# Optimization experiments

Hardware: AMD Instinct MI355X
Metric: run time of the kernel (lower is better)

The kernel has to match this reference:

```python
import jax, jax.numpy as jnp
import numpy as np

S, B, D, CAND = 256, 512, 1024, 1024  # seq_len, batch, mem_dim, cand_dim


def setup_inputs() -> dict:
    key = jax.random.key(0)
    k1, k2, k3, k4 = jax.random.split(key, 4)
    M = jax.random.normal(k1, (S, B, D), dtype=jnp.float32)
    x = jax.random.normal(k2, (B, CAND), dtype=jnp.float32)
    mask = jnp.ones((B, S), dtype=jnp.float32)
    W = jax.random.normal(k3, (D, CAND), dtype=jnp.float32) * 0.02  # nn.Linear weight
    b = jax.random.normal(k4, (D,), dtype=jnp.float32) * 0.02
    return {"M": M, "x": x, "mask": mask, "W": W, "b": b}


def reference(M, x, mask, W, b):
    # M: (S, B, D), x: (B, CAND), mask: (B, S)
    x_ = x @ W.T + b                          # (B, D) -- transform(x)
    Mb = jnp.transpose(M, (1, 2, 0))          # (B, D, S) -- M.permute(1,2,0)
    Mm = Mb * mask[:, None, :]                # mask memory along seq
    alpha_ = jnp.einsum('bd,bds->bs', x_, Mm) * mask  # (B, S) scores, masked
    alpha_ = jnp.tanh(alpha_)
    alpha_ = jax.nn.softmax(alpha_, axis=1)
    am = alpha_ * mask                        # re-mask after softmax
    alpha = am / jnp.sum(am, axis=1, keepdims=True)   # renormalize
    attn_pool = jnp.einsum('bs,sbd->bd', alpha, M)    # (B, D)
    return attn_pool, alpha[:, None, :]       # alpha as (B, 1, S) like torch
```

## Files before the change

### kernel.cpp

```cpp
#include <hip/hip_runtime.h>
#include <hip/hip_bf16.h>
#include <math.h>

#define S_LEN 256
#define B_SZ  512
#define D_DIM 1024
#define CAND_ 1024

#define TB 32
#define TD 64
#define TK 32

__launch_bounds__(256, 2)
__global__ void transform_gemm(const float* __restrict__ x,
                               const float* __restrict__ W,
                               const float* __restrict__ bias,
                               float* __restrict__ xw) {
    __shared__ float xt[TK][TB + 2];
    __shared__ float wt[TK][TD + 4];

    const int b0 = blockIdx.x * TB;
    const int d0 = blockIdx.y * TD;
    const int t  = threadIdx.x;
    const int td = t & 15;
    const int tb = t >> 4;

    float acc0[4] = {0.f, 0.f, 0.f, 0.f};
    float acc1[4] = {0.f, 0.f, 0.f, 0.f};

    const int xr  = t >> 3;
    const int xkc = t & 7;

    for (int k0 = 0; k0 < CAND_; k0 += TK) {
        {
            float4 xv = *(const float4*)&x[(size_t)(b0 + xr) * CAND_ + k0 + xkc * 4];
            xt[xkc * 4 + 0][xr] = xv.x;
            xt[xkc * 4 + 1][xr] = xv.y;
            xt[xkc * 4 + 2][xr] = xv.z;
            xt[xkc * 4 + 3][xr] = xv.w;
        }
        #pragma unroll
        for (int h = 0; h < 2; ++h) {
            int c   = t + h * 256;
            int wr  = c >> 3;
            int wkc = c & 7;
            float4 wv = *(const float4*)&W[(size_t)(d0 + wr) * CAND_ + k0 + wkc * 4];
            wt[wkc * 4 + 0][wr] = wv.x;
            wt[wkc * 4 + 1][wr] = wv.y;
            wt[wkc * 4 + 2][wr] = wv.z;
            wt[wkc * 4 + 3][wr] = wv.w;
        }
        __syncthreads();
        #pragma unroll
        for (int k = 0; k < TK; ++k) {
            float2 xa = *(const float2*)&xt[k][tb * 2];
            float4 wv = *(const float4*)&wt[k][td * 4];
            acc0[0] = fmaf(xa.x, wv.x, acc0[0]);
            acc0[1] = fmaf(xa.x, wv.y, acc0[1]);
            acc0[2] = fmaf(xa.x, wv.z, acc0[2]);
            acc0[3] = fmaf(xa.x, wv.w, acc0[3]);
            acc1[0] = fmaf(xa.y, wv.x, acc1[0]);
            acc1[1] = fmaf(xa.y, wv.y, acc1[1]);
            acc1[2] = fmaf(xa.y, wv.z, acc1[2]);
            acc1[3] = fmaf(xa.y, wv.w, acc1[3]);
        }
        __syncthreads();
    }

    const float4 bv = *(const float4*)&bias[d0 + td * 4];
    const int b = b0 + tb * 2;
    const int d = d0 + td * 4;
    float4 o0 = {acc0[0] + bv.x, acc0[1] + bv.y, acc0[2] + bv.z, acc0[3] + bv.w};
    float4 o1 = {acc1[0] + bv.x, acc1[1] + bv.y, acc1[2] + bv.z, acc1[3] + bv.w};
    *(float4*)&xw[(size_t)b * D_DIM + d]       = o0;
    *(float4*)&xw[(size_t)(b + 1) * D_DIM + d] = o1;
}

#define NW 8
#define NS (S_LEN / NW)

__launch_bounds__(512, 2)
__global__ void fused_attn(const float* __restrict__ M,
                           const float* __restrict__ mask,
                           const float* __restrict__ xw,
                           float* __restrict__ out) {
    __shared__ float s_acc[NW][D_DIM];
    __shared__ float s_w[S_LEN];
    __shared__ float s_den[NW];

    const int b    = blockIdx.x;
    const int tid  = threadIdx.x;
    const int lane = tid & 63;
    const int wv   = tid >> 6;

    const float4* xp = (const float4*)(xw + (size_t)b * D_DIM);
    const float4 x0 = xp[lane];
    const float4 x1 = xp[lane + 64];
    const float4 x2 = xp[lane + 128];
    const float4 x3 = xp[lane + 192];

    const float* mrow = mask + (size_t)b * S_LEN;

    float4 a0 = {0, 0, 0, 0}, a1 = {0, 0, 0, 0}, a2 = {0, 0, 0, 0}, a3 = {0, 0, 0, 0};
    float denom = 0.f;

    const int s_begin = wv * NS;
    const float4* rp = (const float4*)(M + ((size_t)s_begin * B_SZ + b) * D_DIM);
    float4 c0 = rp[lane];
    float4 c1 = rp[lane + 64];
    float4 c2 = rp[lane + 128];
    float4 c3 = rp[lane + 192];

    for (int i = 0; i < NS; ++i) {
        const int s = s_begin + i;
        float4 n0 = c0, n1 = c1, n2 = c2, n3 = c3;
        if (i + 1 < NS) {
            const float4* np = (const float4*)(M + ((size_t)(s + 1) * B_SZ + b) * D_DIM);
            n0 = np[lane];
            n1 = np[lane + 64];
            n2 = np[lane + 128];
            n3 = np[lane + 192];
        }
        float p = c0.x * x0.x;
        p = fmaf(c0.y, x0.y, p); p = fmaf(c0.z, x0.z, p); p = fmaf(c0.w, x0.w, p);
        p = fmaf(c1.x, x1.x, p); p = fmaf(c1.y, x1.y, p); p = fmaf(c1.z, x1.z, p);
        p = fmaf(c1.w, x1.w, p); p = fmaf(c2.x, x2.x, p); p = fmaf(c2.y, x2.y, p);
        p = fmaf(c2.z, x2.z, p); p = fmaf(c2.w, x2.w, p); p = fmaf(c3.x, x3.x, p);
        p = fmaf(c3.y, x3.y, p); p = fmaf(c3.z, x3.z, p); p = fmaf(c3.w, x3.w, p);
        #pragma unroll
        for (int off = 32; off > 0; off >>= 1)
            p += __shfl_xor(p, off, 64);

        const float mk    = mrow[s];
        const float score = p * mk * mk;
        const float w     = mk * expf(tanhf(score));
        denom += w;
        if (lane == 0) s_w[s] = w;

        a0.x = fmaf(w, c0.x, a0.x); a0.y = fmaf(w, c0.y, a0.y);
        a0.z = fmaf(w, c0.z, a0.z); a0.w = fmaf(w, c0.w, a0.w);
        a1.x = fmaf(w, c1.x, a1.x); a1.y = fmaf(w, c1.y, a1.y);
        a1.z = fmaf(w, c1.z, a1.z); a1.w = fmaf(w, c1.w, a1.w);
        a2.x = fmaf(w, c2.x, a2.x); a2.y = fmaf(w, c2.y, a2.y);
        a2.z = fmaf(w, c2.z, a2.z); a2.w = fmaf(w, c2.w, a2.w);
        a3.x = fmaf(w, c3.x, a3.x); a3.y = fmaf(w, c3.y, a3.y);
        a3.z = fmaf(w, c3.z, a3.z); a3.w = fmaf(w, c3.w, a3.w);

        c0 = n0; c1 = n1; c2 = n2; c3 = n3;
    }

    float* sa = &s_acc[wv][0];
    ((float4*)sa)[lane]       = a0;
    ((float4*)sa)[lane + 64]  = a1;
    ((float4*)sa)[lane + 128] = a2;
    ((float4*)sa)[lane + 192] = a3;
    if (lane == 0) s_den[wv] = denom;
    __syncthreads();

    float dtot = 0.f;
    #pragma unroll
    for (int w8 = 0; w8 < NW; ++w8) dtot += s_den[w8];
    const float inv = 1.0f / dtot;

    #pragma unroll
    for (int j = 0; j < 2; ++j) {
        const int d = tid * 2 + j;
        float v = 0.f;
        #pragma unroll
        for (int w8 = 0; w8 < NW; ++w8) v += s_acc[w8][d];
        out[(size_t)b * D_DIM + d] = v * inv;
    }
    if (tid < S_LEN) {
        out[(size_t)B_SZ * D_DIM + (size_t)b * S_LEN + tid] = s_w[tid] * inv;
    }
}

extern "C" void kernel_launch(void* const* d_in, const int* in_sizes, int n_in,
                              void* d_out, int out_size, void* d_ws, size_t ws_size,
                              hipStream_t stream) {
    const float* M    = (const float*)d_in[0];
    const float* x    = (const float*)d_in[1];
    const float* mask = (const float*)d_in[2];
    const float* W    = (const float*)d_in[3];
    const float* bias = (const float*)d_in[4];
    float* out = (float*)d_out;

    const size_t xw_bytes = (size_t)B_SZ * D_DIM * sizeof(float);
    float* xw = (ws_size >= xw_bytes) ? (float*)d_ws : out;

    dim3 ggrid(B_SZ / TB, D_DIM / TD);
    transform_gemm<<<ggrid, 256, 0, stream>>>(x, W, bias, xw);
    fused_attn<<<B_SZ, 512, 0, stream>>>(M, mask, xw, out);
}
```

Baseline: 729.5 us.

## Split-K the transform GEMM and unroll attention loop to two rows per step

The transform GEMM is split along K into two partial outputs written to workspace, which doubles grid parallelism. The attention kernel sums the two partials when it loads x. The attention loop now handles two sequence rows per iteration with independent dot-product chains and interleaved shuffle reductions. The mask is staged in shared memory and launch bounds are raised to four blocks per CU. This raises register pressure from double-buffering eight float4 rows and adds a second partial-buffer write and read.

Result: slower. 754.7 us (+3.5%).

```diff
diff --git a/kernel.cpp b/kernel.cpp
--- a/kernel.cpp
+++ b/kernel.cpp
@@ -15,12 +15,17 @@
 __global__ void transform_gemm(const float* __restrict__ x,
                                const float* __restrict__ W,
                                const float* __restrict__ bias,
-                               float* __restrict__ xw) {
+                               float* __restrict__ xwp,
+                               int ksplit) {
     __shared__ float xt[TK][TB + 2];
     __shared__ float wt[TK][TD + 4];
 
     const int b0 = blockIdx.x * TB;
     const int d0 = blockIdx.y * TD;
+    const int kz = blockIdx.z;
+    const int kspan = CAND_ / ksplit;
+    const int kbase = kz * kspan;
+
     const int t  = threadIdx.x;
     const int td = t & 15;
     const int tb = t >> 4;
@@ -31,7 +36,7 @@
     const int xr  = t >> 3;
     const int xkc = t & 7;
 
-    for (int k0 = 0; k0 < CAND_; k0 += TK) {
+    for (int k0 = kbase; k0 < kbase + kspan; k0 += TK) {
         {
             float4 xv = *(const float4*)&x[(size_t)(b0 + xr) * CAND_ + k0 + xkc * 4];
             xt[xkc * 4 + 0][xr] = xv.x;
@@ -67,25 +72,63 @@
         __syncthreads();
     }
 
-    const float4 bv = *(const float4*)&bias[d0 + td * 4];
+    float bx = 0.f, by = 0.f, bz = 0.f, bw = 0.f;
+    if (kz == 0) {
+        const float4 bv = *(const float4*)&bias[d0 + td * 4];
+        bx = bv.x; by = bv.y; bz = bv.z; bw = bv.w;
+    }
     const int b = b0 + tb * 2;
     const int d = d0 + td * 4;
-    float4 o0 = {acc0[0] + bv.x, acc0[1] + bv.y, acc0[2] + bv.z, acc0[3] + bv.w};
-    float4 o1 = {acc1[0] + bv.x, acc1[1] + bv.y, acc1[2] + bv.z, acc1[3] + bv.w};
-    *(float4*)&xw[(size_t)b * D_DIM + d]       = o0;
-    *(float4*)&xw[(size_t)(b + 1) * D_DIM + d] = o1;
+    float* dst = xwp + (size_t)kz * B_SZ * D_DIM;
+    float4 o0 = {acc0[0] + bx, acc0[1] + by, acc0[2] + bz, acc0[3] + bw};
+    float4 o1 = {acc1[0] + bx, acc1[1] + by, acc1[2] + bz, acc1[3] + bw};
+    *(float4*)&dst[(size_t)b * D_DIM + d]       = o0;
+    *(float4*)&dst[(size_t)(b + 1) * D_DIM + d] = o1;
 }
 
 #define NW 8
 #define NS (S_LEN / NW)
 
-__launch_bounds__(512, 2)
+#define LOAD_ROW(r0, r1, r2, r3, sidx)                                        \
+    do {                                                                      \
+        const float4* _p = (const float4*)(M + ((size_t)(sidx) * B_SZ + b) * D_DIM); \
+        r0 = _p[lane]; r1 = _p[lane + 64]; r2 = _p[lane + 128]; r3 = _p[lane + 192]; \
+    } while (0)
+
+#define DOT4(res, r0, r1, r2, r3)                                             \
+    do {                                                                      \
+        float _p0 = r0.x * x0.x; _p0 = fmaf(r0.y, x0.y, _p0);                 \
+        _p0 = fmaf(r0.z, x0.z, _p0); _p0 = fmaf(r0.w, x0.w, _p0);             \
+        float _p1 = r1.x * x1.x; _p1 = fmaf(r1.y, x1.y, _p1);                 \
+        _p1 = fmaf(r1.z, x1.z, _p1); _p1 = fmaf(r1.w, x1.w, _p1);             \
+        float _p2 = r2.x * x2.x; _p2 = fmaf(r2.y, x2.y, _p2);                 \
+        _p2 = fmaf(r2.z, x2.z, _p2); _p2 = fmaf(r2.w, x2.w, _p2);             \
+        float _p3 = r3.x * x3.x; _p3 = fmaf(r3.y, x3.y, _p3);                 \
+        _p3 = fmaf(r3.z, x3.z, _p3); _p3 = fmaf(r3.w, x3.w, _p3);             \
+        res = (_p0 + _p1) + (_p2 + _p3);                                      \
+    } while (0)
+
+#define ACCW(wgt, r0, r1, r2, r3)                                             \
+    do {                                                                      \
+        a0.x = fmaf(wgt, r0.x, a0.x); a0.y = fmaf(wgt, r0.y, a0.y);           \
+        a0.z = fmaf(wgt, r0.z, a0.z); a0.w = fmaf(wgt, r0.w, a0.w);           \
+        a1.x = fmaf(wgt, r1.x, a1.x); a1.y = fmaf(wgt, r1.y, a1.y);           \
+        a1.z = fmaf(wgt, r1.z, a1.z); a1.w = fmaf(wgt, r1.w, a1.w);           \
+        a2.x = fmaf(wgt, r2.x, a2.x); a2.y = fmaf(wgt, r2.y, a2.y);           \
+        a2.z = fmaf(wgt, r2.z, a2.z); a2.w = fmaf(wgt, r2.w, a2.w);           \
+        a3.x = fmaf(wgt, r3.x, a3.x); a3.y = fmaf(wgt, r3.y, a3.y);           \
+        a3.z = fmaf(wgt, r3.z, a3.z); a3.w = fmaf(wgt, r3.w, a3.w);           \
+    } while (0)
+
+__launch_bounds__(512, 4)
 __global__ void fused_attn(const float* __restrict__ M,
                            const float* __restrict__ mask,
-                           const float* __restrict__ xw,
+                           const float* __restrict__ xw0,
+                           const float* __restrict__ xw1,
                            float* __restrict__ out) {
     __shared__ float s_acc[NW][D_DIM];
     __shared__ float s_w[S_LEN];
+    __shared__ float s_mask[S_LEN];
     __shared__ float s_den[NW];
 
     const int b    = blockIdx.x;
@@ -93,60 +136,62 @@
     const int lane = tid & 63;
     const int wv   = tid >> 6;
 
-    const float4* xp = (const float4*)(xw + (size_t)b * D_DIM);
-    const float4 x0 = xp[lane];
-    const float4 x1 = xp[lane + 64];
-    const float4 x2 = xp[lane + 128];
-    const float4 x3 = xp[lane + 192];
-
-    const float* mrow = mask + (size_t)b * S_LEN;
+    if (tid < S_LEN) s_mask[tid] = mask[(size_t)b * S_LEN + tid];
+
+    const float4* xp0 = (const float4*)(xw0 + (size_t)b * D_DIM);
+    float4 x0 = xp0[lane];
+    float4 x1 = xp0[lane + 64];
+    float4 x2 = xp0[lane + 128];
+    float4 x3 = xp0[lane + 192];
+    if (xw1) {
+        const float4* xp1 = (const float4*)(xw1 + (size_t)b * D_DIM);
+        float4 y0 = xp1[lane], y1 = xp1[lane + 64], y2 = xp1[lane + 128], y3 = xp1[lane + 192];
+        x0.x += y0.x; x0.y += y0.y; x0.z += y0.z; x0.w += y0.w;
+        x1.x += y1.x; x1.y += y1.y; x1.z += y1.z; x1.w += y1.w;
+        x2.x += y2.x; x2.y += y2.y; x2.z += y2.z; x2.w += y2.w;
+        x3.x += y3.x; x3.y += y3.y; x3.z += y3.z; x3.w += y3.w;
+    }
+    __syncthreads();
 
     float4 a0 = {0, 0, 0, 0}, a1 = {0, 0, 0, 0}, a2 = {0, 0, 0, 0}, a3 = {0, 0, 0, 0};
     float denom = 0.f;
 
     const int s_begin = wv * NS;
-    const float4* rp = (const float4*)(M + ((size_t)s_begin * B_SZ + b) * D_DIM);
-    float4 c0 = rp[lane];
-    float4 c1 = rp[lane + 64];
-    float4 c2 = rp[lane + 128];
-    float4 c3 = rp[lane + 192];
-
-    for (int i = 0; i < NS; ++i) {
-        const int s = s_begin + i;
-        float4 n0 = c0, n1 = c1, n2 = c2, n3 = c3;
-        if (i + 1 < NS) {
-            const float4* np = (const float4*)(M + ((size_t)(s + 1) * B_SZ + b) * D_DIM);
-            n0 = np[lane];
-            n1 = np[lane + 64];
-            n2 = np[lane + 128];
-            n3 = np[lane + 192];
-        }
-        float p = c0.x * x0.x;
-        p = fmaf(c0.y, x0.y, p); p = fmaf(c0.z, x0.z, p); p = fmaf(c0.w, x0.w, p);
-        p = fmaf(c1.x, x1.x, p); p = fmaf(c1.y, x1.y, p); p = fmaf(c1.z, x1.z, p);
-        p = fmaf(c1.w, x1.w, p); p = fmaf(c2.x, x2.x, p); p = fmaf(c2.y, x2.y, p);
-        p = fmaf(c2.z, x2.z, p); p = fmaf(c2.w, x2.w, p); p = fmaf(c3.x, x3.x, p);
-        p = fmaf(c3.y, x3.y, p); p = fmaf(c3.z, x3.z, p); p = fmaf(c3.w, x3.w, p);
-        #pragma unroll
-        for (int off = 32; off > 0; off >>= 1)
+    float4 c00, c01, c02, c03, c10, c11, c12, c13;
+    LOAD_ROW(c00, c01, c02, c03, s_begin + 0);
+    LOAD_ROW(c10, c11, c12, c13, s_begin + 1);
+
+    #pragma unroll 2
+    for (int i = 0; i < NS; i += 2) {
+        float4 n00, n01, n02, n03, n10, n11, n12, n13;
+        const bool more = (i + 2 < NS);
+        if (more) {
+            LOAD_ROW(n00, n01, n02, n03, s_begin + i + 2);
+            LOAD_ROW(n10, n11, n12, n13, s_begin + i + 3);
+        }
+        float p, q;
+        DOT4(p, c00, c01, c02, c03);
+        DOT4(q, c10, c11, c12, c13);
+        #pragma unroll
+        for (int off = 32; off > 0; off >>= 1) {
             p += __shfl_xor(p, off, 64);
-
-        const float mk    = mrow[s];
-        const float score = p * mk * mk;
-        const float w     = mk * expf(tanhf(score));
-        denom += w;
-        if (lane == 0) s_w[s] = w;
-
-        a0.x = fmaf(w, c0.x, a0.x); a0.y = fmaf(w, c0.y, a0.y);
-        a0.z = fmaf(w, c0.z, a0.z); a0.w = fmaf(w, c0.w, a0.w);
-        a1.x = fmaf(w, c1.x, a1.x); a1.y = fmaf(w, c1.y, a1.y);
-        a1.z = fmaf(w, c1.z, a1.z); a1.w = fmaf(w, c1.w, a1.w);
-        a2.x = fmaf(w, c2.x, a2.x); a2.y = fmaf(w, c2.y, a2.y);
-        a2.z = fmaf(w, c2.z, a2.z); a2.w = fmaf(w, c2.w, a2.w);
-        a3.x = fmaf(w, c3.x, a3.x); a3.y = fmaf(w, c3.y, a3.y);
-        a3.z = fmaf(w, c3.z, a3.z); a3.w = fmaf(w, c3.w, a3.w);
-
-        c0 = n0; c1 = n1; c2 = n2; c3 = n3;
+            q += __shfl_xor(q, off, 64);
+        }
+        const float mk0 = s_mask[s_begin + i];
+        const float mk1 = s_mask[s_begin + i + 1];
+        const float w0 = mk0 * expf(tanhf(p * mk0 * mk0));
+        const float w1 = mk1 * expf(tanhf(q * mk1 * mk1));
+        denom += w0 + w1;
+        if (lane == 0) {
+            s_w[s_begin + i]     = w0;
+            s_w[s_begin + i + 1] = w1;
+        }
+        ACCW(w0, c00, c01, c02, c03);
+        ACCW(w1, c10, c11, c12, c13);
+        if (more) {
+            c00 = n00; c01 = n01; c02 = n02; c03 = n03;
+            c10 = n10; c11 = n11; c12 = n12; c13 = n13;
+        }
     }
 
     float* sa = &s_acc[wv][0];
@@ -178,6 +223,7 @@
 extern "C" void kernel_launch(void* const* d_in, const int* in_sizes, int n_in,
                               void* d_out, int out_size, void* d_ws, size_t ws_size,
                               hipStream_t stream) {
+    (void)in_sizes; (void)n_in; (void)out_size;
     const float* M    = (const float*)d_in[0];
     const float* x    = (const float*)d_in[1];
     const float* mask = (const float*)d_in[2];
@@ -186,9 +232,14 @@
     float* out = (float*)d_out;
 
     const size_t xw_bytes = (size_t)B_SZ * D_DIM * sizeof(float);
-    float* xw = (ws_size >= xw_bytes) ? (float*)d_ws : out;
-
-    dim3 ggrid(B_SZ / TB, D_DIM / TD);
-    transform_gemm<<<ggrid, 256, 0, stream>>>(x, W, bias, xw);
-    fused_attn<<<B_SZ, 512, 0, stream>>>(M, mask, xw, out);
+    if (ws_size >= 2 * xw_bytes) {
+        float* xwp = (float*)d_ws;
+        dim3 g(B_SZ / TB, D_DIM / TD, 2);
+        transform_gemm<<<g, 256, 0, stream>>>(x, W, bias, xwp, 2);
+        fused_attn<<<B_SZ, 512, 0, stream>>>(M, mask, xwp, xwp + (size_t)B_SZ * D_DIM, out);
+    } else {
+        dim3 g(B_SZ / TB, D_DIM / TD, 1);
+        transform_gemm<<<g, 256, 0, stream>>>(x, W, bias, out, 1);
+        fused_attn<<<B_SZ, 512, 0, stream>>>(M, mask, out, nullptr, out);
+    }
 }
```
